# Kernel optimization log

Hardware: AMD Instinct MI355X
Metric: run time of the kernel (lower is better)

Reference implementation:

```python
import jax, jax.numpy as jnp
import numpy as np

D_MODEL, N_HEADS, D_FF = 1024, 16, 4096
D_K = D_MODEL // N_HEADS
EPS = 1e-5


def layer_norm(x, alpha, beta):
    # torch: unbiased std (ddof=1), divide by (std + eps), scalar alpha/beta
    mean = jnp.mean(x, axis=-1, keepdims=True)
    d = x.shape[-1]
    var = jnp.sum((x - mean) ** 2, axis=-1, keepdims=True) / (d - 1)
    std = jnp.sqrt(var)
    return alpha * (x - mean) / (std + EPS) + beta


def linear(x, w, b):
    # torch nn.Linear: y = x @ W.T + b, W: [out, in]
    return jnp.einsum('bsd,od->bso', x, w) + b


def setup_inputs() -> dict:
    key = jax.random.key(0)
    ks = jax.random.split(key, 12)
    B, S = 4, 2048
    s = 1.0 / np.sqrt(D_MODEL)
    inp = {
        'x': jax.random.normal(ks[0], (B, S, D_MODEL), jnp.float32),
        'mask': jnp.ones((1, 1, 1, S), jnp.bool_),
        'wq': jax.random.normal(ks[1], (D_MODEL, D_MODEL), jnp.float32) * s,
        'bq': jnp.zeros((D_MODEL,), jnp.float32),
        'wk': jax.random.normal(ks[2], (D_MODEL, D_MODEL), jnp.float32) * s,
        'bk': jnp.zeros((D_MODEL,), jnp.float32),
        'wv': jax.random.normal(ks[3], (D_MODEL, D_MODEL), jnp.float32) * s,
        'bv': jnp.zeros((D_MODEL,), jnp.float32),
        'wo': jax.random.normal(ks[4], (D_MODEL, D_MODEL), jnp.float32) * s,
        'bo': jnp.zeros((D_MODEL,), jnp.float32),
        'w1': jax.random.normal(ks[5], (D_FF, D_MODEL), jnp.float32) * s,
        'b1': jnp.zeros((D_FF,), jnp.float32),
        'w2': jax.random.normal(ks[6], (D_MODEL, D_FF), jnp.float32) * (1.0 / np.sqrt(D_FF)),
        'b2': jnp.zeros((D_MODEL,), jnp.float32),
        'ln1_a': jnp.ones((1,), jnp.float32),
        'ln1_b': jnp.zeros((1,), jnp.float32),
        'ln2_a': jnp.ones((1,), jnp.float32),
        'ln2_b': jnp.zeros((1,), jnp.float32),
    }
    return inp


def reference(x, mask, wq, bq, wk, bk, wv, bv, wo, bo, w1, b1, w2, b2,
              ln1_a, ln1_b, ln2_a, ln2_b):
    B, S, _ = x.shape
    # --- residual 1: x + MHA(LN(x)) ---
    h = layer_norm(x, ln1_a, ln1_b)
    q = linear(h, wq, bq).reshape(B, S, N_HEADS, D_K).transpose(0, 2, 1, 3)
    k = linear(h, wk, bk).reshape(B, S, N_HEADS, D_K).transpose(0, 2, 1, 3)
    v = linear(h, wv, bv).reshape(B, S, N_HEADS, D_K).transpose(0, 2, 1, 3)
    score = jnp.einsum('bhqd,bhkd->bhqk', q, k) / jnp.sqrt(jnp.float32(D_K))
    score = jnp.where(mask, score, jnp.float32(-1e9))
    attn = jax.nn.softmax(score, axis=-1)
    ctx = jnp.einsum('bhqk,bhkd->bhqd', attn, v)
    ctx = ctx.transpose(0, 2, 1, 3).reshape(B, S, D_MODEL)
    x = x + linear(ctx, wo, bo)
    # --- residual 2: x + FFN(LN(x)) ---
    h = layer_norm(x, ln2_a, ln2_b)
    h = jax.nn.relu(linear(h, w1, b1))
    x = x + linear(h, w2, b2)
    return x
```

## Files before the change

kernel.cpp:

```cpp
#include <hip/hip_runtime.h>

typedef _Float16 f16;
typedef _Float16 f16x8 __attribute__((ext_vector_type(8)));
typedef _Float16 f16x4 __attribute__((ext_vector_type(4)));
typedef _Float16 f16x2 __attribute__((ext_vector_type(2)));
typedef float f32x4 __attribute__((ext_vector_type(4)));

#define B_ 4
#define S_ 2048
#define DM 1024
#define NH 16
#define DK 64
#define DFF 4096

#define QSCALE 0.18033688011112042f
#define EXPC  -8.656170245333781f

__device__ __forceinline__ void async_copy16(const f16* g, f16* l) {
    __builtin_amdgcn_global_load_lds((const __attribute__((address_space(1))) void*)g,
                                     (__attribute__((address_space(3))) void*)l,
                                     16, 0, 0);
}

__device__ __forceinline__ f16x2 pk_cvt(float a, float b) {
    return __builtin_bit_cast(f16x2, __builtin_amdgcn_cvt_pkrtz(a, b));
}

__global__ __launch_bounds__(256) void convert_all(
        const float* __restrict__ wq, const float* __restrict__ wk,
        const float* __restrict__ wv, const float* __restrict__ wo,
        const float* __restrict__ w1, const float* __restrict__ w2,
        const float* __restrict__ bq, const float* __restrict__ bk,
        const float* __restrict__ bv,
        f16* __restrict__ wqkvb, f16* __restrict__ wob,
        f16* __restrict__ w1b, f16* __restrict__ w2b,
        float* __restrict__ bqkv,
        const float* __restrict__ x, f16* __restrict__ hbuf,
        const float* __restrict__ ln1a, const float* __restrict__ ln1b) {
    const int id = blockIdx.x;
    const int t = threadIdx.x;
    if (id >= 12300) {
        const int row = id - 12300;
        const float4 v = ((const float4*)(x + (size_t)row * DM))[t];
        float s1 = v.x + v.y + v.z + v.w;
        float s2 = v.x * v.x + v.y * v.y + v.z * v.z + v.w * v.w;
        #pragma unroll
        for (int off = 1; off < 64; off <<= 1) {
            s1 += __shfl_xor(s1, off);
            s2 += __shfl_xor(s2, off);
        }
        __shared__ float red[8];
        const int w = t >> 6, lane = t & 63;
        if (lane == 0) { red[w] = s1; red[4 + w] = s2; }
        __syncthreads();
        s1 = red[0] + red[1] + red[2] + red[3];
        s2 = red[4] + red[5] + red[6] + red[7];
        const float mean = s1 * (1.0f / DM);
        const float var = (s2 - s1 * mean) * (1.0f / (DM - 1));
        const float inv = ln1a[0] / (sqrtf(var) + 1e-5f);
        const float beta = ln1b[0];
        f16x4 o = { (f16)((v.x - mean) * inv + beta), (f16)((v.y - mean) * inv + beta),
                    (f16)((v.z - mean) * inv + beta), (f16)((v.w - mean) * inv + beta) };
        ((f16x4*)(hbuf + (size_t)row * DM))[t] = o;
        return;
    }
    const float* src; f16* dst; int base;
    if (id < 1024)      { src = wq; dst = wqkvb;               base = id; }
    else if (id < 2048) { src = wk; dst = wqkvb + 1024 * 1024; base = id - 1024; }
    else if (id < 3072) { src = wv; dst = wqkvb + 2048 * 1024; base = id - 2048; }
    else if (id < 4096) { src = wo; dst = wob;                 base = id - 3072; }
    else if (id < 8192) { src = w1; dst = w1b;                 base = id - 4096; }
    else if (id < 12288){ src = w2; dst = w2b;                 base = id - 8192; }
    else {
        const int i = (id - 12288) * 256 + t;
        if (i < 1024) bqkv[i] = bq[i];
        else if (i < 2048) bqkv[i] = bk[i - 1024];
        else if (i < 3072) bqkv[i] = bv[i - 2048];
        return;
    }
    const int i = base * 256 + t;
    float4 v = ((const float4*)src)[i];
    f16x4 o = { (f16)v.x, (f16)v.y, (f16)v.z, (f16)v.w };
    ((f16x4*)dst)[i] = o;
}

__global__ __launch_bounds__(256) void ln_kernel(const float* __restrict__ x,
                                                 f16* __restrict__ out,
                                                 const float* __restrict__ alpha_p,
                                                 const float* __restrict__ beta_p) {
    const int row = blockIdx.x;
    const int t = threadIdx.x;
    const float4 v = ((const float4*)(x + (size_t)row * DM))[t];
    float s1 = v.x + v.y + v.z + v.w;
    float s2 = v.x * v.x + v.y * v.y + v.z * v.z + v.w * v.w;
    #pragma unroll
    for (int off = 1; off < 64; off <<= 1) {
        s1 += __shfl_xor(s1, off);
        s2 += __shfl_xor(s2, off);
    }
    __shared__ float red[8];
    const int w = t >> 6, lane = t & 63;
    if (lane == 0) { red[w] = s1; red[4 + w] = s2; }
    __syncthreads();
    s1 = red[0] + red[1] + red[2] + red[3];
    s2 = red[4] + red[5] + red[6] + red[7];
    const float mean = s1 * (1.0f / DM);
    const float var = (s2 - s1 * mean) * (1.0f / (DM - 1));
    const float inv = alpha_p[0] / (sqrtf(var) + 1e-5f);
    const float beta = beta_p[0];
    f16x4 o = { (f16)((v.x - mean) * inv + beta), (f16)((v.y - mean) * inv + beta),
                (f16)((v.z - mean) * inv + beta), (f16)((v.w - mean) * inv + beta) };
    ((f16x4*)(out + (size_t)row * DM))[t] = o;
}

template <int MODE, int BK = 32>
__global__ __launch_bounds__(256, 2) void gemm_bt(const f16* __restrict__ A,
                                                  const f16* __restrict__ B,
                                                  const float* __restrict__ bias,
                                                  const float* __restrict__ resid,
                                                  void* __restrict__ Cout,
                                                  f16* __restrict__ vT,
                                                  int M, int N, int K) {
    __shared__ __align__(16) f16 SMEM[4][128 * BK];
    const int t = threadIdx.x;
    const int lane = t & 63;
    const int w = t >> 6;
    const int quad = lane >> 4;
    const int l15 = lane & 15;
    const int wm = (w >> 1) * 64, wn = (w & 1) * 64;

    const int gx = gridDim.x;
    const int nwg = gx * gridDim.y;
    int lin = blockIdx.y * gx + blockIdx.x;
    lin = (lin & 7) * (nwg >> 3) + (lin >> 3);
    const int bm = (lin / gx) * 128, bn = (lin % gx) * 128;

    f32x4 acc[4][4];
    #pragma unroll
    for (int i = 0; i < 4; ++i)
        #pragma unroll
        for (int j = 0; j < 4; ++j)
            acc[i][j] = (f32x4){0.f, 0.f, 0.f, 0.f};

    int arow, csw;
    if constexpr (BK == 32) {
        arow = t >> 2;
        csw = ((t & 3) ^ ((arow >> 1) & 3)) * 8;
    } else {
        arow = t >> 3;
        csw = ((t & 7) ^ (arow & 7)) * 8;
    }
    const f16* Ag = A + (size_t)(bm + arow) * K + csw;
    const f16* Bg = B + (size_t)(bn + arow) * K + csw;
    const int wbase = (t & ~63) * 8;

    auto stage = [&](int ktile, int buf) {
        const f16* Agk = Ag + ktile * BK;
        const f16* Bgk = Bg + ktile * BK;
        if constexpr (BK == 32) {
            async_copy16(Agk,                  &SMEM[buf][wbase]);
            async_copy16(Agk + (size_t)64 * K, &SMEM[buf][2048 + wbase]);
            async_copy16(Bgk,                  &SMEM[2 + buf][wbase]);
            async_copy16(Bgk + (size_t)64 * K, &SMEM[2 + buf][2048 + wbase]);
        } else {
            #pragma unroll
            for (int g = 0; g < 4; ++g) {
                async_copy16(Agk + (size_t)(g * 32) * K, &SMEM[buf][g * 2048 + wbase]);
                async_copy16(Bgk + (size_t)(g * 32) * K, &SMEM[2 + buf][g * 2048 + wbase]);
            }
        }
    };

    stage(0, 0);
    __syncthreads();

    const int nkt = K / BK;
    for (int kt = 0; kt < nkt; ++kt) {
        const int cur = kt & 1;
        if (kt + 1 < nkt) stage(kt + 1, cur ^ 1);

        if constexpr (BK == 32) {
            f16x8 af[4], bf[4];
            #pragma unroll
            for (int mt = 0; mt < 4; ++mt) {
                const int r = wm + mt * 16 + l15;
                const int slot = quad ^ ((r >> 1) & 3);
                af[mt] = *(const f16x8*)&SMEM[cur][r * 32 + slot * 8];
            }
            #pragma unroll
            for (int nt = 0; nt < 4; ++nt) {
                const int r = wn + nt * 16 + l15;
                const int slot = quad ^ ((r >> 1) & 3);
                bf[nt] = *(const f16x8*)&SMEM[2 + cur][r * 32 + slot * 8];
            }
            #pragma unroll
            for (int mt = 0; mt < 4; ++mt)
                #pragma unroll
                for (int nt = 0; nt < 4; ++nt)
                    acc[mt][nt] = __builtin_amdgcn_mfma_f32_16x16x32_f16(af[mt], bf[nt], acc[mt][nt], 0, 0, 0);
        } else {
            #pragma unroll
            for (int half = 0; half < 2; ++half) {
                f16x8 af[4], bf[4];
                #pragma unroll
                for (int mt = 0; mt < 4; ++mt) {
                    const int r = wm + mt * 16 + l15;
                    const int slot = (quad + half * 4) ^ (r & 7);
                    af[mt] = *(const f16x8*)&SMEM[cur][r * 64 + slot * 8];
                }
                #pragma unroll
                for (int nt = 0; nt < 4; ++nt) {
                    const int r = wn + nt * 16 + l15;
                    const int slot = (quad + half * 4) ^ (r & 7);
                    bf[nt] = *(const f16x8*)&SMEM[2 + cur][r * 64 + slot * 8];
                }
                #pragma unroll
                for (int mt = 0; mt < 4; ++mt)
                    #pragma unroll
                    for (int nt = 0; nt < 4; ++nt)
                        acc[mt][nt] = __builtin_amdgcn_mfma_f32_16x16x32_f16(af[mt], bf[nt], acc[mt][nt], 0, 0, 0);
            }
        }

        __syncthreads();
    }

    const int r0 = bm + wm + (quad * 4);
    const int c0 = bn + wn + l15;

    if constexpr (MODE == 2) {
        #pragma unroll
        for (int mt = 0; mt < 4; ++mt)
            #pragma unroll
            for (int nt = 0; nt < 4; ++nt) {
                const int col = c0 + nt * 16;
                const float bv = bias[col];
                #pragma unroll
                for (int i = 0; i < 4; ++i) {
                    const int row = r0 + mt * 16 + i;
                    ((float*)Cout)[(size_t)row * N + col] =
                        acc[mt][nt][i] + bv + resid[(size_t)row * N + col];
                }
            }
        return;
    }

    if (MODE == 3 && bn >= 2048) {
        #pragma unroll
        for (int mt = 0; mt < 4; ++mt)
            #pragma unroll
            for (int nt = 0; nt < 4; ++nt) {
                const int col = c0 + nt * 16;
                const float bv = bias[col];
                const int h = (col >> 6) & 15;
                const int d = col & 63;
                const int rowb = r0 + mt * 16;
                const int b = rowb >> 11, s = rowb & 2047;
                f16x4 pk;
                #pragma unroll
                for (int i = 0; i < 4; ++i) pk[i] = (f16)(acc[mt][nt][i] + bv);
                *(f16x4*)&vT[(size_t)(((b << 4) + h) * 64 + d) * 2048 + s] = pk;
            }
        return;
    }

    static_assert(BK == 64 || MODE == 2, "LDS epilogue sized for BK=64");
    {
        constexpr int CST = 136;
        f16* Cs = &SMEM[0][0];
        const float qs = (MODE == 3 && bn < 1024) ? QSCALE : 1.f;
        #pragma unroll
        for (int mt = 0; mt < 4; ++mt)
            #pragma unroll
            for (int nt = 0; nt < 4; ++nt) {
                const int lcol = wn + nt * 16 + l15;
                const float bv = bias[bn + lcol];
                #pragma unroll
                for (int i = 0; i < 4; ++i) {
                    const int lrow = wm + mt * 16 + quad * 4 + i;
                    float v = acc[mt][nt][i] + bv;
                    if (MODE == 1) v = v > 0.f ? v : 0.f;
                    Cs[lrow * CST + lcol] = (f16)(v * qs);
                }
            }
        __syncthreads();
        #pragma unroll
        for (int k = 0; k < 8; ++k) {
            const int e = t * 8 + k * 2048;
            const int row = e >> 7, colg = e & 127;
            const f16x8 vv = *(const f16x8*)&Cs[row * CST + colg];
            *(f16x8*)&((f16*)Cout)[(size_t)(bm + row) * N + bn + colg] = vv;
        }
    }
}

__global__ __launch_bounds__(256, 4) void attn_kernel(const f16* __restrict__ qkv,
                                                      const f16* __restrict__ vT,
                                                      f16* __restrict__ ctx) {
    const int lin = blockIdx.y * 16 + blockIdx.x;
    const int xcd = lin & 7, idx = lin >> 3;
    const int bh = (idx >> 4) * 8 + xcd;
    const int q0 = (idx & 15) * 128;
    const int b = bh >> 4, h = bh & 15;
    const int t = threadIdx.x, lane = t & 63, w = t >> 6;
    const int quad = lane >> 4, l15 = lane & 15;
    const int e = l15 & 7;

    __shared__ __align__(16) f16 KV[4][64 * 64];

    const int srow = t >> 3;
    const int scS = ((t & 7) ^ (srow & 7)) * 8;

    const f16* Kg = qkv + (size_t)(b * S_ + srow) * 3072 + 1024 + h * 64 + scS;
    const f16* Vg = vT + (size_t)(bh * 64 + srow) * S_ + scS;
    const int wb8 = (t & ~63) * 8;

    {
        const f16* g = qkv + (size_t)(b * S_ + q0 + srow) * 3072 + h * 64 + scS;
        f16* dst = &KV[0][wb8];
        #pragma unroll
        for (int c = 0; c < 4; ++c)
            async_copy16(g + (size_t)(c * 32) * 3072, dst + c * 2048);
    }
    __syncthreads();

    f16x8 qf[2][2];
    #pragma unroll
    for (int band = 0; band < 2; ++band) {
        const int qr = w * 32 + band * 16 + l15;
        const int qx = qr & 7;
        qf[band][0] = *(const f16x8*)&KV[0][qr * 64 + ((quad) ^ qx) * 8];
        qf[band][1] = *(const f16x8*)&KV[0][qr * 64 + ((quad + 4) ^ qx) * 8];
    }
    __syncthreads();

    {
        async_copy16(Kg, &KV[0][wb8]);
        async_copy16(Kg + (size_t)32 * 3072, &KV[0][2048 + wb8]);
        async_copy16(Vg, &KV[2][wb8]);
        async_copy16(Vg + (size_t)32 * S_, &KV[2][2048 + wb8]);
    }
    __syncthreads();

    const int kbase0 = l15 * 64 + ((quad) ^ e) * 8;
    const int kbase1 = l15 * 64 + ((quad + 4) ^ e) * 8;
    int vbase[4];
    #pragma unroll
    for (int kb = 0; kb < 4; ++kb)
        vbase[kb] = l15 * 64 + (((kb * 2) + (quad >> 1)) ^ e) * 8 + (quad & 1) * 4;

    const f16 one = (f16)1.f;
    const f16x4 ones4 = { one, one, one, one };
    const f32x4 einit = (f32x4){EXPC, EXPC, EXPC, EXPC};

    f32x4 o[2][4];
    f32x4 accl[2];
    #pragma unroll
    for (int band = 0; band < 2; ++band) {
        accl[band] = (f32x4){0.f, 0.f, 0.f, 0.f};
        #pragma unroll
        for (int dt = 0; dt < 4; ++dt) o[band][dt] = (f32x4){0.f, 0.f, 0.f, 0.f};
    }

    for (int j = 0; j < 32; ++j) {
        const int cur = j & 1;
        if (j + 1 < 32) {
            const int nxt = cur ^ 1;
            const f16* kg = Kg + (size_t)(j + 1) * 64 * 3072;
            async_copy16(kg, &KV[nxt][wb8]);
            async_copy16(kg + (size_t)32 * 3072, &KV[nxt][2048 + wb8]);
            const f16* vg = Vg + (j + 1) * 64;
            async_copy16(vg, &KV[2 + nxt][wb8]);
            async_copy16(vg + (size_t)32 * S_, &KV[2 + nxt][2048 + wb8]);
        }

        f16x4 pa[2][4];
        #pragma unroll
        for (int band = 0; band < 2; ++band) {
            #pragma unroll
            for (int nt = 0; nt < 4; ++nt) {
                const f16x8 kf0 = *(const f16x8*)&KV[cur][kbase0 + nt * 1024];
                const f16x8 kf1 = *(const f16x8*)&KV[cur][kbase1 + nt * 1024];
                f32x4 s = einit;
                s = __builtin_amdgcn_mfma_f32_16x16x32_f16(kf0, qf[band][0], s, 0, 0, 0);
                s = __builtin_amdgcn_mfma_f32_16x16x32_f16(kf1, qf[band][1], s, 0, 0, 0);
                const f16x2 lo = pk_cvt(__builtin_amdgcn_exp2f(s[0]),
                                        __builtin_amdgcn_exp2f(s[1]));
                const f16x2 hi = pk_cvt(__builtin_amdgcn_exp2f(s[2]),
                                        __builtin_amdgcn_exp2f(s[3]));
                const f16x4 p = __builtin_shufflevector(lo, hi, 0, 1, 2, 3);
                pa[band][nt] = p;
                accl[band] = __builtin_amdgcn_mfma_f32_16x16x16f16(p, ones4, accl[band], 0, 0, 0);
            }
        }

        __builtin_amdgcn_s_setprio(1);
        #pragma unroll
        for (int dt = 0; dt < 4; ++dt) {
            #pragma unroll
            for (int kb = 0; kb < 4; ++kb) {
                const f16x4 vf = *(const f16x4*)&KV[2 + cur][vbase[kb] + dt * 1024];
                o[0][dt] = __builtin_amdgcn_mfma_f32_16x16x16f16(pa[0][kb], vf, o[0][dt], 0, 0, 0);
                o[1][dt] = __builtin_amdgcn_mfma_f32_16x16x16f16(pa[1][kb], vf, o[1][dt], 0, 0, 0);
            }
        }
        __builtin_amdgcn_s_setprio(0);

        __syncthreads();
    }

    #pragma unroll
    for (int band = 0; band < 2; ++band) {
        float linv[4];
        #pragma unroll
        for (int i = 0; i < 4; ++i) linv[i] = 1.f / accl[band][i];
        #pragma unroll
        for (int dt = 0; dt < 4; ++dt)
            #pragma unroll
            for (int i = 0; i < 4; ++i) {
                const int r = q0 + w * 32 + band * 16 + quad * 4 + i;
                const int d = dt * 16 + l15;
                ctx[(size_t)(b * S_ + r) * DM + h * 64 + d] = (f16)(o[band][dt][i] * linv[i]);
            }
    }
}

extern "C" void kernel_launch(void* const* d_in, const int* in_sizes, int n_in,
                              void* d_out, int out_size, void* d_ws, size_t ws_size,
                              hipStream_t stream) {
    const float* x    = (const float*)d_in[0];
    const float* wq   = (const float*)d_in[2];
    const float* bq   = (const float*)d_in[3];
    const float* wk   = (const float*)d_in[4];
    const float* bk   = (const float*)d_in[5];
    const float* wv   = (const float*)d_in[6];
    const float* bv   = (const float*)d_in[7];
    const float* wo   = (const float*)d_in[8];
    const float* bo   = (const float*)d_in[9];
    const float* w1   = (const float*)d_in[10];
    const float* b1   = (const float*)d_in[11];
    const float* w2   = (const float*)d_in[12];
    const float* b2   = (const float*)d_in[13];
    const float* ln1a = (const float*)d_in[14];
    const float* ln1b = (const float*)d_in[15];
    const float* ln2a = (const float*)d_in[16];
    const float* ln2b = (const float*)d_in[17];
    float* out = (float*)d_out;

    char* ws = (char*)d_ws;
    size_t off = 0;
    auto alloc = [&](size_t bytes) -> void* {
        void* p = ws + off;
        off += (bytes + 255) & ~(size_t)255;
        return p;
    };
    f16* wqkvb  = (f16*)alloc((size_t)3072 * 1024 * 2);
    f16* wob    = (f16*)alloc((size_t)1024 * 1024 * 2);
    f16* w1b    = (f16*)alloc((size_t)4096 * 1024 * 2);
    f16* w2b    = (f16*)alloc((size_t)1024 * 4096 * 2);
    float* bqkv = (float*)alloc((size_t)3072 * 4);
    f16* hbuf   = (f16*)alloc((size_t)8192 * 1024 * 2);
    f16* qkvb   = (f16*)alloc((size_t)8192 * 3072 * 2);
    f16* vTb    = (f16*)alloc((size_t)64 * 64 * 2048 * 2);
    f16* ctxb   = (f16*)alloc((size_t)8192 * 1024 * 2);
    f16* ffn1b  = qkvb;

    const int M = B_ * S_;

    convert_all<<<12300 + M, 256, 0, stream>>>(wq, wk, wv, wo, w1, w2, bq, bk, bv,
                                               wqkvb, wob, w1b, w2b, bqkv,
                                               x, hbuf, ln1a, ln1b);
    gemm_bt<3, 64><<<dim3(3072 / 128, M / 128), 256, 0, stream>>>(hbuf, wqkvb, bqkv, nullptr, qkvb, vTb, M, 3072, 1024);
    attn_kernel<<<dim3(16, 64), 256, 0, stream>>>(qkvb, vTb, ctxb);
    gemm_bt<2, 64><<<dim3(1024 / 128, M / 128), 256, 0, stream>>>(ctxb, wob, bo, x, out, nullptr, M, 1024, 1024);
    ln_kernel<<<M, 256, 0, stream>>>(out, hbuf, ln2a, ln2b);
    gemm_bt<1, 64><<<dim3(4096 / 128, M / 128), 256, 0, stream>>>(hbuf, w1b, b1, nullptr, ffn1b, nullptr, M, 4096, 1024);
    gemm_bt<2, 64><<<dim3(1024 / 128, M / 128), 256, 0, stream>>>(ffn1b, w2b, b2, out, out, nullptr, M, 1024, 4096);
}
```

Before: 492.6 us.

## Add 256x256-tile 8-wave pipelined GEMM for FFN1 with ReLU epilogue

Introduces a new GEMM kernel with 256x256 output tiles, 512 threads, and a double-buffered LDS pipeline. Each K-step is split into four MFMA phases, with async global-to-LDS loads for the next tile interleaved between them. It also remaps blocks in XCD-aware order and uses XOR-swizzled LDS addressing. The kernel replaces the 128x128 gemm_bt for the FFN1 projection to raise arithmetic intensity and overlap loads with compute. The cost is 128KB of LDS per block and a large accumulator register footprint, which limit occupancy to about 2 blocks.

```diff
diff --git a/kernel.cpp b/kernel.cpp
--- a/kernel.cpp
+++ b/kernel.cpp
@@ -291,6 +291,126 @@
             const f16x8 vv = *(const f16x8*)&Cs[row * CST + colg];
             *(f16x8*)&((f16*)Cout)[(size_t)(bm + row) * N + bn + colg] = vv;
         }
+    }
+}
+
+__global__ __launch_bounds__(512, 2) void gemm_8ph(const f16* __restrict__ A,
+                                                   const f16* __restrict__ B,
+                                                   const float* __restrict__ bias,
+                                                   f16* __restrict__ Cout,
+                                                   int M, int N, int K) {
+    __shared__ __align__(16) f16 SM[65536];
+    const int t = threadIdx.x;
+    const int lane = t & 63, w = t >> 6;
+    const int quad = lane >> 4, l15 = lane & 15;
+    const int wm = (w >> 2) * 128, wn = (w & 3) * 64;
+
+    const int gx = gridDim.x;
+    const int nwg = gx * gridDim.y;
+    int lin = blockIdx.y * gx + blockIdx.x;
+    lin = (lin & 7) * (nwg >> 3) + (lin >> 3);
+    const int bm = (lin / gx) * 256, bn = (lin % gx) * 256;
+
+    f32x4 acc[8][4];
+    #pragma unroll
+    for (int i = 0; i < 8; ++i)
+        #pragma unroll
+        for (int j = 0; j < 4; ++j)
+            acc[i][j] = (f32x4){0.f, 0.f, 0.f, 0.f};
+
+    const int rt = t >> 3;
+    const int csw = ((t & 7) ^ (rt & 7)) * 8;
+    const f16* Ag = A + (size_t)(bm + rt) * K + csw;
+    const f16* Bg = B + (size_t)(bn + rt) * K + csw;
+    const int wb8 = (t & ~63) * 8;
+
+    auto issue = [&](int kt, int hh, int isB) {
+        const f16* g = (isB ? Bg : Ag) + (size_t)(hh * 64) * K + kt * 64;
+        f16* d = &SM[(isB ? 32768 : 0) + (kt & 1) * 16384 + hh * 4096 + wb8];
+        async_copy16(g, d);
+    };
+
+    auto phase = [&](int cb, int mh, int nh) {
+        f16x8 af[4][2], bf[2][2];
+        #pragma unroll
+        for (int mt = 0; mt < 4; ++mt) {
+            const int r = wm + mh * 64 + mt * 16 + l15;
+            #pragma unroll
+            for (int kp = 0; kp < 2; ++kp) {
+                const int slot = (quad + kp * 4) ^ (r & 7);
+                af[mt][kp] = *(const f16x8*)&SM[cb * 16384 + r * 64 + slot * 8];
+            }
+        }
+        #pragma unroll
+        for (int nf = 0; nf < 2; ++nf) {
+            const int r = wn + nh * 32 + nf * 16 + l15;
+            #pragma unroll
+            for (int kp = 0; kp < 2; ++kp) {
+                const int slot = (quad + kp * 4) ^ (r & 7);
+                bf[nf][kp] = *(const f16x8*)&SM[32768 + cb * 16384 + r * 64 + slot * 8];
+            }
+        }
+        __builtin_amdgcn_s_setprio(1);
+        #pragma unroll
+        for (int mt = 0; mt < 4; ++mt)
+            #pragma unroll
+            for (int nf = 0; nf < 2; ++nf)
+                #pragma unroll
+                for (int kp = 0; kp < 2; ++kp)
+                    acc[mh * 4 + mt][nh * 2 + nf] = __builtin_amdgcn_mfma_f32_16x16x32_f16(
+                        af[mt][kp], bf[nf][kp], acc[mh * 4 + mt][nh * 2 + nf], 0, 0, 0);
+        __builtin_amdgcn_s_setprio(0);
+    };
+
+    #pragma unroll
+    for (int hh = 0; hh < 4; ++hh) issue(0, hh, 1);
+    #pragma unroll
+    for (int hh = 0; hh < 4; ++hh) issue(0, hh, 0);
+    asm volatile("s_waitcnt vmcnt(0)" ::: "memory");
+    __builtin_amdgcn_s_barrier();
+    asm volatile("" ::: "memory");
+
+    const int nkt = K >> 6;
+    for (int kt = 0; kt < nkt; ++kt) {
+        const int cb = kt & 1;
+        const bool pf = (kt + 1 < nkt);
+        if (pf) { issue(kt + 1, 0, 1); issue(kt + 1, 1, 1); }
+        phase(cb, 0, 0);
+        if (pf) { issue(kt + 1, 2, 1); issue(kt + 1, 3, 1); }
+        phase(cb, 0, 1);
+        asm volatile("s_waitcnt vmcnt(4)" ::: "memory");
+        __builtin_amdgcn_s_barrier();
+        asm volatile("" ::: "memory");
+        if (pf) { issue(kt + 1, 0, 0); issue(kt + 1, 2, 0); }
+        phase(cb, 1, 0);
+        if (pf) { issue(kt + 1, 1, 0); issue(kt + 1, 3, 0); }
+        phase(cb, 1, 1);
+        asm volatile("s_waitcnt vmcnt(2)" ::: "memory");
+        __builtin_amdgcn_s_barrier();
+        asm volatile("" ::: "memory");
+    }
+
+    #pragma unroll
+    for (int am = 0; am < 8; ++am) {
+        const int lrow = wm + (am >> 2) * 64 + (am & 3) * 16 + quad * 4;
+        #pragma unroll
+        for (int an = 0; an < 4; ++an) {
+            const int lcol = wn + (an >> 1) * 32 + (an & 1) * 16 + l15;
+            const float bv = bias[bn + lcol];
+            #pragma unroll
+            for (int i = 0; i < 4; ++i) {
+                float v = acc[am][an][i] + bv;
+                v = v > 0.f ? v : 0.f;
+                SM[(lrow + i) * 256 + lcol] = (f16)v;
+            }
+        }
+    }
+    __syncthreads();
+    #pragma unroll
+    for (int k = 0; k < 16; ++k) {
+        const int e = t * 8 + k * 4096;
+        const int row = e >> 8, col = e & 255;
+        *(f16x8*)&Cout[(size_t)(bm + row) * N + bn + col] = *(const f16x8*)&SM[e];
     }
 }
 
@@ -474,6 +594,6 @@
     attn_kernel<<<dim3(16, 64), 256, 0, stream>>>(qkvb, vTb, ctxb);
     gemm_bt<2, 64><<<dim3(1024 / 128, M / 128), 256, 0, stream>>>(ctxb, wob, bo, x, out, nullptr, M, 1024, 1024);
     ln_kernel<<<M, 256, 0, stream>>>(out, hbuf, ln2a, ln2b);
-    gemm_bt<1, 64><<<dim3(4096 / 128, M / 128), 256, 0, stream>>>(hbuf, w1b, b1, nullptr, ffn1b, nullptr, M, 4096, 1024);
+    gemm_8ph<<<dim3(4096 / 256, M / 256), 512, 0, stream>>>(hbuf, w1b, b1, ffn1b, M, 4096, 1024);
     gemm_bt<2, 64><<<dim3(1024 / 128, M / 128), 256, 0, stream>>>(ffn1b, w2b, b2, out, out, nullptr, M, 1024, 4096);
 }
```

New measurement: 489.7 us. No clear change (-0.6%).
